# Performance work log

Hardware: AMD Instinct MI355X
Metric: run time of the kernel (lower is better)

## Reference

```python
import jax, jax.numpy as jnp
import numpy as np

B, C, H, W = 2, 64, 128, 128

def setup_inputs() -> dict:
    key = jax.random.key(0)
    k1, k2, k3 = jax.random.split(key, 3)
    x = jax.random.normal(k1, (B, C, H, W), dtype=jnp.float32)
    y = jax.random.normal(k2, (B, C, H, W), dtype=jnp.float32)
    z = jax.random.normal(k3, (B, C, H, W), dtype=jnp.float32)
    return {"x": x, "y": y, "z": z}

def reference(x, y, z):
    # x=q, y=k, z=v, all [b,c,h,w]. Per pixel:
    #   kv[i,j] = v[i] * k[j]          (c x c outer product)
    #   attn    = softmax over i (dim=1 in torch, the v axis)
    #   out[i]  = sum_j attn[i,j] * q[j]
    q = jnp.transpose(x, (0, 2, 3, 1))  # [b,h,w,c]
    k = jnp.transpose(y, (0, 2, 3, 1))
    v = jnp.transpose(z, (0, 2, 3, 1))
    kv = v[..., :, None] * k[..., None, :]          # [b,h,w,c,c]
    attn = jax.nn.softmax(kv, axis=-2)              # softmax over v-axis i
    out = jnp.einsum('bhwij,bhwj->bhwi', attn, q)   # [b,h,w,c]
    return jnp.transpose(out, (0, 3, 1, 2))         # [b,c,h,w]
```

## Files before the change

kernel.cpp:

```cpp
#include <hip/hip_runtime.h>


constexpr int C    = 64;
constexpr int HW   = 128 * 128;
constexpr int NPIX = 2 * HW;
constexpr int ICH  = 4;
constexpr int JT   = 8;
constexpr int PXB  = 16;
constexpr int LSTR = 68;
#define LOG2E 1.4426950408889634f

template <int CTRL>
__device__ __forceinline__ float dpp_add(float x) {
  int xi = __builtin_bit_cast(int, x);
  int yi = __builtin_amdgcn_update_dpp(0, xi, CTRL, 0xF, 0xF, true);
  return x + __builtin_bit_cast(float, yi);
}

__global__ __launch_bounds__(256, 6) void channel_mixing_kernel(
    const float* __restrict__ q,
    const float* __restrict__ kk,
    const float* __restrict__ v,
    float* __restrict__ out) {
  __shared__ __align__(16) float lds_k[PXB * LSTR];
  __shared__ __align__(16) float lds_q[PXB * LSTR];

  const int t        = threadIdx.x;
  const int pixblock = blockIdx.x * PXB;
  const int gbase = ((pixblock >> 14) << 20) | (pixblock & (HW - 1));

#pragma unroll
  for (int rep = 0; rep < 4; ++rep) {
    const int idx = rep * 256 + t;
    const int j   = idx >> 4;
    const int pxs = idx & 15;
    lds_k[pxs * LSTR + j] = kk[gbase + (j << 14) + pxs];
    lds_q[pxs * LSTR + j] = q [gbase + (j << 14) + pxs];
  }

  const int lane = t & 63;
  const int p    = lane >> 4;
  const int ig   = lane & 15;
  const int px   = (t >> 6) * 4 + p;
  const int base  = gbase + px;
  const int cbase = base + (ig << 16);

  float vv[ICH];
#pragma unroll
  for (int ii = 0; ii < ICH; ++ii)
    vv[ii] = v[cbase + (ii << 14)] * LOG2E;

  float acc[ICH];
#pragma unroll
  for (int ii = 0; ii < ICH; ++ii) acc[ii] = 0.0f;

  __syncthreads();

  const float* lkp = &lds_k[px * LSTR];
  const float* lqp = &lds_q[px * LSTR];

#pragma unroll 1
  for (int jt = 0; jt < C / JT; ++jt) {
    float kx[JT], qx[JT];
    *(float4*)&kx[0] = *(const float4*)&lkp[jt * JT];
    *(float4*)&kx[4] = *(const float4*)&lkp[jt * JT + 4];
    *(float4*)&qx[0] = *(const float4*)&lqp[jt * JT];
    *(float4*)&qx[4] = *(const float4*)&lqp[jt * JT + 4];

    float e[JT][ICH];
#pragma unroll
    for (int jj = 0; jj < JT; ++jj)
#pragma unroll
      for (int ii = 0; ii < ICH; ++ii)
        e[jj][ii] = __builtin_amdgcn_exp2f(vv[ii] * kx[jj]);

    float S[JT];
#pragma unroll
    for (int jj = 0; jj < JT; ++jj)
      S[jj] = (e[jj][0] + e[jj][1]) + (e[jj][2] + e[jj][3]);
#pragma unroll
    for (int jj = 0; jj < JT; ++jj) S[jj] = dpp_add<0xB1>(S[jj]);
#pragma unroll
    for (int jj = 0; jj < JT; ++jj) S[jj] = dpp_add<0x4E>(S[jj]);
#pragma unroll
    for (int jj = 0; jj < JT; ++jj) S[jj] = dpp_add<0x141>(S[jj]);
#pragma unroll
    for (int jj = 0; jj < JT; ++jj) S[jj] = dpp_add<0x140>(S[jj]);

#pragma unroll
    for (int jj = 0; jj < JT; ++jj) {
      const float w = qx[jj] * __builtin_amdgcn_rcpf(S[jj]);
#pragma unroll
      for (int ii = 0; ii < ICH; ++ii) acc[ii] += w * e[jj][ii];
    }
  }

#pragma unroll
  for (int ii = 0; ii < ICH; ++ii)
    out[cbase + (ii << 14)] = acc[ii];
}

extern "C" void kernel_launch(void* const* d_in, const int* in_sizes, int n_in,
                              void* d_out, int out_size, void* d_ws, size_t ws_size,
                              hipStream_t stream) {
  const float* q  = (const float*)d_in[0];
  const float* kk = (const float*)d_in[1];
  const float* v  = (const float*)d_in[2];
  float* out = (float*)d_out;

  dim3 grid(NPIX / PXB);
  dim3 block(256);
  channel_mixing_kernel<<<grid, block, 0, stream>>>(q, kk, v, out);
}
```

Before: 96.04 us.

## Remap threads to eight channels per lane with 32-pixel blocks and prefetch

```diff
diff --git a/kernel.cpp b/kernel.cpp
--- a/kernel.cpp
+++ b/kernel.cpp
@@ -4,9 +4,8 @@
 constexpr int C    = 64;
 constexpr int HW   = 128 * 128;
 constexpr int NPIX = 2 * HW;
-constexpr int ICH  = 4;
-constexpr int JT   = 8;
-constexpr int PXB  = 16;
+constexpr int JT   = 4;
+constexpr int PXB  = 32;
 constexpr int LSTR = 68;
 #define LOG2E 1.4426950408889634f
 
@@ -17,7 +16,7 @@
   return x + __builtin_bit_cast(float, yi);
 }
 
-__global__ __launch_bounds__(256, 6) void channel_mixing_kernel(
+__global__ __launch_bounds__(256, 4) void channel_mixing_kernel(
     const float* __restrict__ q,
     const float* __restrict__ kk,
     const float* __restrict__ v,
@@ -29,75 +28,99 @@
   const int pixblock = blockIdx.x * PXB;
   const int gbase = ((pixblock >> 14) << 20) | (pixblock & (HW - 1));
 
+  const int lane = t & 63;
+  const int p    = lane >> 3;
+  const int ig   = lane & 7;
+  const int px   = (t >> 6) * 8 + p;
+  const int base  = gbase + px;
+  const int cbase = base + (ig << 17);
+
+  float2 vv2[4];
 #pragma unroll
-  for (int rep = 0; rep < 4; ++rep) {
-    const int idx = rep * 256 + t;
-    const int j   = idx >> 4;
-    const int pxs = idx & 15;
-    lds_k[pxs * LSTR + j] = kk[gbase + (j << 14) + pxs];
-    lds_q[pxs * LSTR + j] = q [gbase + (j << 14) + pxs];
+  for (int n = 0; n < 4; ++n) {
+    float a = v[cbase + ((2 * n) << 14)];
+    float b = v[cbase + ((2 * n + 1) << 14)];
+    vv2[n] = make_float2(a * LOG2E, b * LOG2E);
   }
 
-  const int lane = t & 63;
-  const int p    = lane >> 4;
-  const int ig   = lane & 15;
-  const int px   = (t >> 6) * 4 + p;
-  const int base  = gbase + px;
-  const int cbase = base + (ig << 16);
+#pragma unroll
+  for (int rep = 0; rep < 2; ++rep) {
+    const int s  = rep * 256 + t;
+    const int j  = s >> 3;
+    const int pg = (s & 7) * 4;
+    float4 k4 = *(const float4*)&kk[gbase + (j << 14) + pg];
+    float4 q4 = *(const float4*)&q [gbase + (j << 14) + pg];
+    lds_k[(pg + 0) * LSTR + j] = k4.x;  lds_q[(pg + 0) * LSTR + j] = q4.x;
+    lds_k[(pg + 1) * LSTR + j] = k4.y;  lds_q[(pg + 1) * LSTR + j] = q4.y;
+    lds_k[(pg + 2) * LSTR + j] = k4.z;  lds_q[(pg + 2) * LSTR + j] = q4.z;
+    lds_k[(pg + 3) * LSTR + j] = k4.w;  lds_q[(pg + 3) * LSTR + j] = q4.w;
+  }
 
-  float vv[ICH];
+  float2 acc2[4];
 #pragma unroll
-  for (int ii = 0; ii < ICH; ++ii)
-    vv[ii] = v[cbase + (ii << 14)] * LOG2E;
-
-  float acc[ICH];
-#pragma unroll
-  for (int ii = 0; ii < ICH; ++ii) acc[ii] = 0.0f;
+  for (int n = 0; n < 4; ++n) acc2[n] = make_float2(0.0f, 0.0f);
 
   __syncthreads();
 
-  const float* lkp = &lds_k[px * LSTR];
-  const float* lqp = &lds_q[px * LSTR];
+  const float4* lkp4 = (const float4*)&lds_k[px * LSTR];
+  const float4* lqp4 = (const float4*)&lds_q[px * LSTR];
+
+  float4 kx4 = lkp4[0];
+  float4 qx4 = lqp4[0];
 
 #pragma unroll 1
   for (int jt = 0; jt < C / JT; ++jt) {
-    float kx[JT], qx[JT];
-    *(float4*)&kx[0] = *(const float4*)&lkp[jt * JT];
-    *(float4*)&kx[4] = *(const float4*)&lkp[jt * JT + 4];
-    *(float4*)&qx[0] = *(const float4*)&lqp[jt * JT];
-    *(float4*)&qx[4] = *(const float4*)&lqp[jt * JT + 4];
+    const int nxt = (jt < C / JT - 1) ? jt + 1 : jt;
+    float4 kxn = lkp4[nxt];
+    float4 qxn = lqp4[nxt];
 
-    float e[JT][ICH];
+    const float kx[JT] = {kx4.x, kx4.y, kx4.z, kx4.w};
+    const float qx[JT] = {qx4.x, qx4.y, qx4.z, qx4.w};
+
+    float2 e2[JT][4];
 #pragma unroll
     for (int jj = 0; jj < JT; ++jj)
 #pragma unroll
-      for (int ii = 0; ii < ICH; ++ii)
-        e[jj][ii] = __builtin_amdgcn_exp2f(vv[ii] * kx[jj]);
+      for (int n = 0; n < 4; ++n) {
+        float mx = vv2[n].x * kx[jj];
+        float my = vv2[n].y * kx[jj];
+        e2[jj][n] = make_float2(__builtin_amdgcn_exp2f(mx),
+                                __builtin_amdgcn_exp2f(my));
+      }
 
     float S[JT];
 #pragma unroll
-    for (int jj = 0; jj < JT; ++jj)
-      S[jj] = (e[jj][0] + e[jj][1]) + (e[jj][2] + e[jj][3]);
+    for (int jj = 0; jj < JT; ++jj) {
+      float2 s2 = make_float2((e2[jj][0].x + e2[jj][1].x) + (e2[jj][2].x + e2[jj][3].x),
+                              (e2[jj][0].y + e2[jj][1].y) + (e2[jj][2].y + e2[jj][3].y));
+      S[jj] = s2.x + s2.y;
+    }
 #pragma unroll
     for (int jj = 0; jj < JT; ++jj) S[jj] = dpp_add<0xB1>(S[jj]);
 #pragma unroll
     for (int jj = 0; jj < JT; ++jj) S[jj] = dpp_add<0x4E>(S[jj]);
 #pragma unroll
     for (int jj = 0; jj < JT; ++jj) S[jj] = dpp_add<0x141>(S[jj]);
-#pragma unroll
-    for (int jj = 0; jj < JT; ++jj) S[jj] = dpp_add<0x140>(S[jj]);
 
 #pragma unroll
     for (int jj = 0; jj < JT; ++jj) {
       const float w = qx[jj] * __builtin_amdgcn_rcpf(S[jj]);
 #pragma unroll
-      for (int ii = 0; ii < ICH; ++ii) acc[ii] += w * e[jj][ii];
+      for (int n = 0; n < 4; ++n) {
+        acc2[n].x += w * e2[jj][n].x;
+        acc2[n].y += w * e2[jj][n].y;
+      }
     }
+
+    kx4 = kxn;
+    qx4 = qxn;
   }
 
 #pragma unroll
-  for (int ii = 0; ii < ICH; ++ii)
-    out[cbase + (ii << 14)] = acc[ii];
+  for (int n = 0; n < 4; ++n) {
+    out[cbase + ((2 * n) << 14)]     = acc2[n].x;
+    out[cbase + ((2 * n + 1) << 14)] = acc2[n].y;
+  }
 }
 
 extern "C" void kernel_launch(void* const* d_in, const int* in_sizes, int n_in,
```

After: 89.64 us. -6.7%, faster.
